# Kernel tuning notes

Hardware: AMD Instinct MI355X
Metric: run time of the kernel (lower is better)

The kernel has to match this reference:

```python
import jax, jax.numpy as jnp
import numpy as np

S, T, B = 128, 64, 64          # src_len, trg_len, batch
E, H, D, A, V = 512, 512, 1024, 256, 32000  # emb, enc_hid, dec_hid(=2H), attn, vocab
PAD = 0


def _p(key, shape, scale=0.02):
    return jax.random.normal(key, shape, dtype=jnp.float32) * scale


def setup_inputs() -> dict:
    key = jax.random.key(0)
    ks = jax.random.split(key, 20)
    return {
        'src': jax.random.randint(ks[0], (S, B), 0, V, dtype=jnp.int32),
        'trg': jax.random.randint(ks[1], (T, B), 0, V, dtype=jnp.int32),
        'enc_emb': _p(ks[2], (V, E)),
        'Wf_ih': _p(ks[3], (4 * H, E)), 'Wf_hh': _p(ks[4], (4 * H, H)), 'bf': jnp.zeros((4 * H,), jnp.float32),
        'Wb_ih': _p(ks[5], (4 * H, E)), 'Wb_hh': _p(ks[6], (4 * H, H)), 'bb': jnp.zeros((4 * H,), jnp.float32),
        'Wa': _p(ks[7], (A, 2 * H + D)), 'ba': jnp.zeros((A,), jnp.float32),
        'v': _p(ks[8], (A,)),
        'dec_emb': _p(ks[9], (V, E)),
        'Wd_ih': _p(ks[10], (4 * D, E + 2 * H)), 'Wd_hh': _p(ks[11], (4 * D, D)), 'bd': jnp.zeros((4 * D,), jnp.float32),
        'Wo': _p(ks[12], (V, 2 * H + D + E)), 'bo': jnp.zeros((V,), jnp.float32),
    }


def lstm_cell(x, h, c, W_ih, W_hh, b):
    # PyTorch gate order: i, f, g, o
    g = x @ W_ih.T + h @ W_hh.T + b
    i, f, gg, o = jnp.split(g, 4, axis=-1)
    c2 = jax.nn.sigmoid(f) * c + jax.nn.sigmoid(i) * jnp.tanh(gg)
    h2 = jax.nn.sigmoid(o) * jnp.tanh(c2)
    return h2, c2


def seq2seq_fwd(src, trg, enc_emb, Wf_ih, Wf_hh, bf, Wb_ih, Wb_hh, bb,
                Wa, ba, v, dec_emb, Wd_ih, Wd_hh, bd, Wo, bo):
    emb = enc_emb[src]                                   # [S,B,E]
    z = jnp.zeros((B, H), emb.dtype)

    def fstep(carry, x):
        h, c = lstm_cell(x, *carry, Wf_ih, Wf_hh, bf)
        return (h, c), h

    def bstep(carry, x):
        h, c = lstm_cell(x, *carry, Wb_ih, Wb_hh, bb)
        return (h, c), h

    (hf, cf), hs_f = jax.lax.scan(fstep, (z, z), emb)
    (hb, cb), hs_b = jax.lax.scan(bstep, (z, z), emb[::-1])
    enc_out = jnp.concatenate([hs_f, hs_b[::-1]], axis=-1)   # [S,B,2H]

    h0 = jnp.concatenate([hf, hb], axis=-1)              # [B,D]
    c0 = jnp.concatenate([cf, cb], axis=-1)

    mask = (src != PAD).T                                # [B,S]
    enc_bse = enc_out.transpose(1, 0, 2)                 # [B,S,2H]

    def dstep(carry, tok):
        h, c = carry
        emb_t = dec_emb[tok]                             # [B,E]
        hrep = jnp.broadcast_to(h[:, None, :], (B, S, D))
        energy = jnp.tanh(jnp.concatenate([hrep, enc_bse], -1) @ Wa.T + ba)  # [B,S,A]
        scores = energy @ v                              # [B,S]
        scores = jnp.where(mask, scores, jnp.float32(-1e10))
        a = jax.nn.softmax(scores, axis=1)
        ctx = jnp.einsum('bs,bse->be', a, enc_bse)       # [B,2H]
        x = jnp.concatenate([emb_t, ctx], axis=-1)
        h2, c2 = lstm_cell(x, h, c, Wd_ih, Wd_hh, bd)
        pred = jnp.concatenate([h2, ctx, emb_t], -1) @ Wo.T + bo  # [B,V]
        return (h2, c2), pred

    # teacher_forcing_ratio = 1.0 -> input at step t is trg[t-1]
    _, preds = jax.lax.scan(dstep, (h0, c0), trg[:-1])
    outputs = jnp.concatenate([jnp.zeros((1, B, V), preds.dtype), preds], axis=0)
    return outputs                                       # [T,B,V]


def reference(src, trg, enc_emb, Wf_ih, Wf_hh, bf, Wb_ih, Wb_hh, bb,
              Wa, ba, v, dec_emb, Wd_ih, Wd_hh, bd, Wo, bo):
    return seq2seq_fwd(src, trg, enc_emb, Wf_ih, Wf_hh, bf, Wb_ih, Wb_hh, bb,
                       Wa, ba, v, dec_emb, Wd_ih, Wd_hh, bd, Wo, bo)
```

## Files before the change

kernel.cpp:

```cpp
#include <hip/hip_runtime.h>

#define SLEN  128
#define BATCH 64
#define EMB   512
#define HID   512
#define DDEC  1024
#define ATT   256
#define VOC   32000
#define TSTEPS 63
#define LINE  16

typedef _Float16 f16x4 __attribute__((ext_vector_type(4)));
typedef _Float16 f16x8 __attribute__((ext_vector_type(8)));
typedef float    f32x4 __attribute__((ext_vector_type(4)));

union HQ  { unsigned long long q[2]; f16x8 v; };
union HP  { _Float16 h[2]; unsigned u; };
union HP4 { _Float16 h[4]; f16x4 v4; unsigned long long u; };

__device__ __forceinline__ float sigmoidf_(float x) { return 1.0f / (1.0f + __expf(-x)); }
__device__ __forceinline__ float tanhf_(float x)    { return 1.0f - 2.0f / (__expf(2.0f * x) + 1.0f); }

__device__ __forceinline__ void st_u32(void* p, unsigned v) {
    __hip_atomic_store((unsigned*)p, v, __ATOMIC_RELAXED, __HIP_MEMORY_SCOPE_AGENT);
}
__device__ __forceinline__ void st_u64(void* p, unsigned long long v) {
    __hip_atomic_store((unsigned long long*)p, v, __ATOMIC_RELAXED, __HIP_MEMORY_SCOPE_AGENT);
}
__device__ __forceinline__ unsigned long long ld_u64(const void* p) {
    return __hip_atomic_load((const unsigned long long*)p, __ATOMIC_RELAXED, __HIP_MEMORY_SCOPE_AGENT);
}

__device__ __forceinline__ void barx(int* base, int leaf, int perleaf, int nleaf) {
    __syncthreads();
    if (threadIdx.x == 0) {
        int* lc = base + leaf * LINE;
        int* lg = base + (16 + leaf) * LINE;
        int* rc = base + 32 * LINE;
        int* rg = base + 33 * LINE;
        int g = __hip_atomic_load(lg, __ATOMIC_RELAXED, __HIP_MEMORY_SCOPE_AGENT);
        int prev = __hip_atomic_fetch_add(lc, 1, __ATOMIC_RELAXED, __HIP_MEMORY_SCOPE_AGENT);
        if (prev == perleaf - 1) {
            __hip_atomic_store(lc, 0, __ATOMIC_RELAXED, __HIP_MEMORY_SCOPE_AGENT);
            int rgen = __hip_atomic_load(rg, __ATOMIC_RELAXED, __HIP_MEMORY_SCOPE_AGENT);
            int rprev = __hip_atomic_fetch_add(rc, 1, __ATOMIC_RELAXED, __HIP_MEMORY_SCOPE_AGENT);
            if (rprev == nleaf - 1) {
                __hip_atomic_store(rc, 0, __ATOMIC_RELAXED, __HIP_MEMORY_SCOPE_AGENT);
                __hip_atomic_store(rg, rgen + 1, __ATOMIC_RELAXED, __HIP_MEMORY_SCOPE_AGENT);
            } else {
                while (__hip_atomic_load(rg, __ATOMIC_RELAXED, __HIP_MEMORY_SCOPE_AGENT) == rgen)
                    __builtin_amdgcn_s_sleep(1);
            }
            __hip_atomic_store(lg, g + 1, __ATOMIC_RELAXED, __HIP_MEMORY_SCOPE_AGENT);
        } else {
            while (__hip_atomic_load(lg, __ATOMIC_RELAXED, __HIP_MEMORY_SCOPE_AGENT) == g)
                __builtin_amdgcn_s_sleep(1);
        }
    }
    __syncthreads();
}

__global__ __launch_bounds__(256) void init_convert(
    const int* __restrict__ src, const int* __restrict__ trg,
    const float* __restrict__ enc_emb, const float* __restrict__ dec_emb,
    const float* __restrict__ Wf_ih, const float* __restrict__ Wf_hh,
    const float* __restrict__ Wb_ih, const float* __restrict__ Wb_hh,
    const float* __restrict__ Wa, const float* __restrict__ Wd_ih, const float* __restrict__ Wd_hh,
    float* __restrict__ out0,
    _Float16* __restrict__ Wenc16, _Float16* __restrict__ Wd16, _Float16* __restrict__ Wa16,
    _Float16* __restrict__ emb_src16, _Float16* __restrict__ predA,
    float* __restrict__ c_enc, _Float16* __restrict__ h16_enc, int* __restrict__ bar_ws)
{
    long idx = (long)blockIdx.x * 256 + threadIdx.x;
    if (idx < 2048000L) { out0[idx] = 0.f; return; }
    idx -= 2048000L;
    if (idx < 4194304L) {
        int dir = (int)(idx >> 21);
        int rem = (int)(idx & ((1 << 21) - 1));
        int rr = rem >> 10, c = rem & 1023;
        int d = rr >> 2, qg = rr & 3;
        const float* Wih = dir ? Wb_ih : Wf_ih;
        const float* Whh = dir ? Wb_hh : Wf_hh;
        float v = (c < 512) ? Wih[(long)(qg * 512 + d) * 512 + c]
                            : Whh[(long)(qg * 512 + d) * 512 + (c - 512)];
        Wenc16[idx] = (_Float16)v; return;
    }
    idx -= 4194304L;
    if (idx < 10485760L) {
        int rr = (int)(idx / 2560), c = (int)(idx % 2560);
        int d = rr >> 2, qg = rr & 3;
        float v = (c < 1536) ? Wd_ih[(long)(qg * 1024 + d) * 1536 + c]
                             : Wd_hh[(long)(qg * 1024 + d) * 1024 + (c - 1536)];
        Wd16[idx] = (_Float16)v; return;
    }
    idx -= 10485760L;
    if (idx < 262144L) {
        int rr = (int)(idx >> 10), c = (int)(idx & 1023);
        Wa16[idx] = (_Float16)Wa[(long)rr * 2048 + c]; return;
    }
    idx -= 262144L;
    if (idx < 4194304L) {
        int sb = (int)(idx >> 9), e = (int)(idx & 511);
        int tok = src[sb];
        emb_src16[idx] = (_Float16)enc_emb[(long)tok * 512 + e]; return;
    }
    idx -= 4194304L;
    if (idx < 2064384L) {
        int rI = (int)(idx >> 9), e = (int)(idx & 511);
        int tok = trg[rI];
        predA[(long)(64 + rI) * 2560 + 2048 + e] = (_Float16)dec_emb[(long)tok * 512 + e]; return;
    }
    idx -= 2064384L;
    if (idx < 65536L) { c_enc[idx] = 0.f; return; }
    idx -= 65536L;
    if (idx < 65536L) { h16_enc[idx] = (_Float16)0.f; return; }
    idx -= 65536L;
    if (idx < 2048L) { bar_ws[idx] = 0; }
}

__global__ __launch_bounds__(256, 1) void enc_coop(
    const _Float16* __restrict__ Wenc16, const _Float16* __restrict__ emb_src16,
    _Float16* __restrict__ h16_enc, float* __restrict__ c_enc,
    const float* __restrict__ bf, const float* __restrict__ bb,
    _Float16* __restrict__ enc_out16, int* __restrict__ bar_ws)
{
    __shared__ _Float16 Wl[16384];
    __shared__ float gbuf[16][65];

    const int t = threadIdx.x, lane = t & 63, w = t >> 6;
    const int blk = blockIdx.x, dir = blk >> 7, tile = blk & 127;
    const int r16 = lane & 15, kg = lane >> 4;
    int* bar_base = bar_ws + dir * 34 * LINE;
    const int leaf = tile & 15;

    #pragma unroll
    for (int i = 0; i < 8; ++i) {
        int h0 = (i * 256 + t) * 8;
        int kc = h0 >> 9, l = (h0 >> 3) & 63;
        f16x8 v = *(const f16x8*)(Wenc16 + ((size_t)(dir * 2048 + tile * 16 + (l & 15))) * 1024 + (l >> 4) * 8 + kc * 32);
        *(f16x8*)&Wl[h0] = v;
    }

    const float* bias = dir ? bb : bf;
    const int pb = t & 63, pp = (t >> 6) & 1;
    float bias2[2][4];
    float creg2[2] = {0.f, 0.f};
    if (t < 128) {
        #pragma unroll
        for (int j = 0; j < 2; ++j)
            #pragma unroll
            for (int q = 0; q < 4; ++q)
                bias2[j][q] = bias[q * 512 + tile * 4 + pp * 2 + j];
    }
    __syncthreads();

    for (int s = 0; s < SLEN; ++s) {
        const int par = s & 1;
        const int s_eff = dir ? (127 - s) : s;
        const _Float16* Ax = emb_src16 + ((size_t)(s_eff * 64 + w * 16 + r16)) * 512 + kg * 8;
        const unsigned long long* Hq =
            (const unsigned long long*)(h16_enc + ((size_t)((par * 2 + dir) * 64 + w * 16 + r16)) * 512);
        f32x4 a0 = {}, a1 = {};
        #pragma unroll 8
        for (int kc = 0; kc < 16; ++kc) {
            f16x8 bx = *(const f16x8*)&Wl[kc * 512 + lane * 8];
            f16x8 ax = *(const f16x8*)(Ax + kc * 32);
            a0 = __builtin_amdgcn_mfma_f32_16x16x32_f16(ax, bx, a0, 0, 0, 0);
            f16x8 bh = *(const f16x8*)&Wl[(16 + kc) * 512 + lane * 8];
            HQ hq;
            hq.q[0] = ld_u64(Hq + kc * 8 + kg * 2);
            hq.q[1] = ld_u64(Hq + kc * 8 + kg * 2 + 1);
            a1 = __builtin_amdgcn_mfma_f32_16x16x32_f16(hq.v, bh, a1, 0, 0, 0);
        }
        #pragma unroll
        for (int rI = 0; rI < 4; ++rI)
            gbuf[r16][w * 16 + kg * 4 + rI] = a0[rI] + a1[rI];
        __syncthreads();
        if (t < 128) {
            HP hp;
            #pragma unroll
            for (int j = 0; j < 2; ++j) {
                const int dl = pp * 2 + j;
                float g0 = gbuf[dl * 4 + 0][pb] + bias2[j][0];
                float g1 = gbuf[dl * 4 + 1][pb] + bias2[j][1];
                float g2 = gbuf[dl * 4 + 2][pb] + bias2[j][2];
                float g3 = gbuf[dl * 4 + 3][pb] + bias2[j][3];
                float c2 = sigmoidf_(g1) * creg2[j] + sigmoidf_(g0) * tanhf_(g2);
                float h2 = sigmoidf_(g3) * tanhf_(c2);
                creg2[j] = c2;
                hp.h[j] = (_Float16)h2;
            }
            const int d0 = tile * 4 + pp * 2;
            st_u32((void*)(h16_enc + ((size_t)((par ^ 1) * 2 + dir) * 64 + pb) * 512 + d0), hp.u);
            *(unsigned*)(enc_out16 + ((size_t)s_eff * 64 + pb) * 1024 + dir * 512 + d0) = hp.u;
        }
        barx(bar_base, leaf, 8, 16);
    }
    if (t < 128) {
        const int d0 = tile * 4 + pp * 2;
        c_enc[((size_t)dir * 64 + pb) * 512 + d0] = creg2[0];
        c_enc[((size_t)dir * 64 + pb) * 512 + d0 + 1] = creg2[1];
    }
}

__global__ __launch_bounds__(256, 1) void dec_coop(
    const _Float16* __restrict__ Wd16, const _Float16* __restrict__ Wa16,
    const float* __restrict__ bd, const float* __restrict__ vvec,
    const int* __restrict__ src, const _Float16* __restrict__ enc_part16,
    const _Float16* __restrict__ enc_out16, const float* __restrict__ c_enc,
    _Float16* __restrict__ predA, int* __restrict__ bar_ws)
{
    __shared__ _Float16 Wl[40960];
    __shared__ float gbuf[16][65];
    __shared__ float ha[256], sv[256], sc[128], red[128];

    const int t = threadIdx.x, lane = t & 63, w = t >> 6;
    const int tile = blockIdx.x;
    const int r16 = lane & 15, kg = lane >> 4;
    int* bar_base = bar_ws + 2 * 34 * LINE;
    const int leaf = tile & 15;

    #pragma unroll
    for (int i = 0; i < 20; ++i) {
        int h0 = (i * 256 + t) * 8;
        int kc = h0 >> 9, l = (h0 >> 3) & 63;
        f16x8 v = *(const f16x8*)(Wd16 + ((size_t)(tile * 16 + (l & 15))) * 2560 + (l >> 4) * 8 + kc * 32);
        *(f16x8*)&Wl[h0] = v;
    }

    const int pb = t & 63, pp = (t >> 6) & 1;
    float bias2[2][4], creg2[2] = {0.f, 0.f};
    if (t < 128) {
        #pragma unroll
        for (int j = 0; j < 2; ++j) {
            const int dg = tile * 4 + pp * 2 + j;
            #pragma unroll
            for (int q = 0; q < 4; ++q) bias2[j][q] = bd[q * 1024 + dg];
            creg2[j] = (dg < 512) ? c_enc[(size_t)pb * 512 + dg]
                                  : c_enc[(size_t)(64 + pb) * 512 + (dg - 512)];
        }
    }

    const int b0 = blockIdx.x;
    if (b0 < 64) {
        sv[t] = vvec[t];
        #pragma unroll
        for (int i = 0; i < 2; ++i) {
            int pidx = i * 256 + t;
            int d = pidx * 2;
            const size_t rbase = (d < 512) ? (size_t)(127 * 64 + b0) * 1024 : (size_t)(0 * 64 + b0) * 1024;
            HP hp;
            hp.h[0] = enc_out16[rbase + d];
            hp.h[1] = enc_out16[rbase + d + 1];
            st_u32((void*)(predA + (size_t)b0 * 2560 + d), hp.u);
        }
    }
    barx(bar_base, leaf, 16, 16);

    for (int tt = 0; tt < TSTEPS; ++tt) {
        if (b0 < 64) {
            const int base_m = b0 & 48;
            const _Float16* Ahh = predA + ((size_t)(tt * 64 + base_m + r16)) * 2560 + kg * 8;
            f32x4 acc4[4] = {};
            #pragma unroll 4
            for (int kc = 0; kc < 32; ++kc) {
                f16x8 a = *(const f16x8*)(Ahh + kc * 32);
                #pragma unroll
                for (int jj = 0; jj < 4; ++jj) {
                    f16x8 bw = *(const f16x8*)(Wa16 + ((size_t)((w * 4 + jj) * 16 + r16)) * 1024 + kg * 8 + kc * 32);
                    acc4[jj] = __builtin_amdgcn_mfma_f32_16x16x32_f16(a, bw, acc4[jj], 0, 0, 0);
                }
            }
            if (kg == ((b0 & 15) >> 2)) {
                #pragma unroll
                for (int jj = 0; jj < 4; ++jj)
                    ha[(w * 4 + jj) * 16 + r16] = acc4[jj][b0 & 3];
            }
            __syncthreads();
            if (t < 128) {
                const f16x8* ep = (const f16x8*)(enc_part16 + ((size_t)t * 64 + b0) * 256);
                float acc = 0.f;
                #pragma unroll 4
                for (int j8 = 0; j8 < 32; ++j8) {
                    f16x8 e = ep[j8];
                    #pragma unroll
                    for (int u = 0; u < 8; ++u)
                        acc += tanhf_(ha[j8 * 8 + u] + (float)e[u]) * sv[j8 * 8 + u];
                }
                float scv = (src[t * 64 + b0] != 0) ? acc : -1e10f;
                sc[t] = scv; red[t] = scv;
            }
            __syncthreads();
            for (int off = 64; off > 0; off >>= 1) { if (t < off) red[t] = fmaxf(red[t], red[t + off]); __syncthreads(); }
            const float mx = red[0];
            __syncthreads();
            if (t < 128) { float e = __expf(sc[t] - mx); sc[t] = e; red[t] = e; }
            __syncthreads();
            for (int off = 64; off > 0; off >>= 1) { if (t < off) red[t] += red[t + off]; __syncthreads(); }
            const float inv = 1.0f / red[0];
            __syncthreads();
            float a0 = 0.f, a1 = 0.f, a2 = 0.f, a3 = 0.f;
            for (int sI = 0; sI < 128; ++sI) {
                float as = sc[sI] * inv;
                f16x4 ev = *(const f16x4*)(enc_out16 + ((size_t)sI * 64 + b0) * 1024 + t * 4);
                a0 += as * (float)ev[0]; a1 += as * (float)ev[1];
                a2 += as * (float)ev[2]; a3 += as * (float)ev[3];
            }
            HP4 o;
            o.h[0] = (_Float16)a0; o.h[1] = (_Float16)a1;
            o.h[2] = (_Float16)a2; o.h[3] = (_Float16)a3;
            st_u64((void*)(predA + ((size_t)(64 + tt * 64 + b0)) * 2560 + 1024 + t * 4), o.u);
        }
        barx(bar_base, leaf, 16, 16);
        {
            const _Float16* Ae = predA + ((size_t)(64 + tt * 64 + w * 16 + r16)) * 2560 + kg * 8;
            const _Float16* Ah = predA + ((size_t)(tt * 64 + w * 16 + r16)) * 2560 + kg * 8;
            f32x4 ae = {}, ac = {}, ah = {};
            #pragma unroll 8
            for (int kc = 0; kc < 16; ++kc) {
                f16x8 bw = *(const f16x8*)&Wl[kc * 512 + lane * 8];
                f16x8 a = *(const f16x8*)(Ae + 2048 + kc * 32);
                ae = __builtin_amdgcn_mfma_f32_16x16x32_f16(a, bw, ae, 0, 0, 0);
            }
            #pragma unroll 8
            for (int kc = 0; kc < 32; ++kc) {
                f16x8 bw = *(const f16x8*)&Wl[(16 + kc) * 512 + lane * 8];
                f16x8 a = *(const f16x8*)(Ae + 1024 + kc * 32);
                ac = __builtin_amdgcn_mfma_f32_16x16x32_f16(a, bw, ac, 0, 0, 0);
            }
            #pragma unroll 8
            for (int kc = 0; kc < 32; ++kc) {
                f16x8 bw = *(const f16x8*)&Wl[(48 + kc) * 512 + lane * 8];
                f16x8 a = *(const f16x8*)(Ah + kc * 32);
                ah = __builtin_amdgcn_mfma_f32_16x16x32_f16(a, bw, ah, 0, 0, 0);
            }
            #pragma unroll
            for (int rI = 0; rI < 4; ++rI)
                gbuf[r16][w * 16 + kg * 4 + rI] = ae[rI] + ac[rI] + ah[rI];
            __syncthreads();
            if (t < 128) {
                HP hp;
                #pragma unroll
                for (int j = 0; j < 2; ++j) {
                    const int dl = pp * 2 + j;
                    float g0 = gbuf[dl * 4 + 0][pb] + bias2[j][0];
                    float g1 = gbuf[dl * 4 + 1][pb] + bias2[j][1];
                    float g2 = gbuf[dl * 4 + 2][pb] + bias2[j][2];
                    float g3 = gbuf[dl * 4 + 3][pb] + bias2[j][3];
                    float c2 = sigmoidf_(g1) * creg2[j] + sigmoidf_(g0) * tanhf_(g2);
                    float h2 = sigmoidf_(g3) * tanhf_(c2);
                    creg2[j] = c2;
                    hp.h[j] = (_Float16)h2;
                }
                st_u32((void*)(predA + ((size_t)(64 + tt * 64 + pb)) * 2560 + tile * 4 + pp * 2), hp.u);
            }
        }
        barx(bar_base, leaf, 16, 16);
    }
}

__global__ __launch_bounds__(64) void enc_step_mfma(
    const _Float16* __restrict__ Wenc16, const _Float16* __restrict__ emb_src16,
    _Float16* __restrict__ h16_enc, float* __restrict__ c_enc,
    const float* __restrict__ bf, const float* __restrict__ bb,
    _Float16* __restrict__ enc_out16, int s)
{
    __shared__ float gbuf[16 * 66];
    const int lane = threadIdx.x;
    const int blk = blockIdx.x;
    const int dir = blk >> 7, tile = blk & 127;
    const int par = s & 1;
    const int s_eff = dir ? (SLEN - 1 - s) : s;
    const int r16 = lane & 15, kg = lane >> 4;

    const _Float16* Bw = Wenc16 + ((size_t)(dir * 2048 + tile * 16 + r16)) * 1024 + kg * 8;
    const _Float16* Ax = emb_src16 + ((size_t)(s_eff * 64 + r16)) * 512 + kg * 8;
    const _Float16* Ah = h16_enc + ((size_t)((par * 2 + dir) * 64 + r16)) * 512 + kg * 8;

    f32x4 acc[4] = {};
    #pragma unroll 4
    for (int kc = 0; kc < 16; ++kc) {
        f16x8 bfr = *(const f16x8*)(Bw + kc * 32);
        #pragma unroll
        for (int m = 0; m < 4; ++m) {
            f16x8 a = *(const f16x8*)(Ax + kc * 32 + (size_t)m * 16 * 512);
            acc[m] = __builtin_amdgcn_mfma_f32_16x16x32_f16(a, bfr, acc[m], 0, 0, 0);
        }
    }
    #pragma unroll 4
    for (int kc = 0; kc < 16; ++kc) {
        f16x8 bfr = *(const f16x8*)(Bw + 512 + kc * 32);
        #pragma unroll
        for (int m = 0; m < 4; ++m) {
            f16x8 a = *(const f16x8*)(Ah + kc * 32 + (size_t)m * 16 * 512);
            acc[m] = __builtin_amdgcn_mfma_f32_16x16x32_f16(a, bfr, acc[m], 0, 0, 0);
        }
    }
    #pragma unroll
    for (int m = 0; m < 4; ++m)
        #pragma unroll
        for (int rI = 0; rI < 4; ++rI)
            gbuf[r16 * 66 + m * 16 + kg * 4 + rI] = acc[m][rI];
    __syncthreads();

    const float* bias = dir ? bb : bf;
    const int b = lane;
    #pragma unroll
    for (int dl = 0; dl < 4; ++dl) {
        const int d = tile * 4 + dl;
        float g0 = gbuf[(dl * 4 + 0) * 66 + b] + bias[d];
        float g1 = gbuf[(dl * 4 + 1) * 66 + b] + bias[512 + d];
        float g2 = gbuf[(dl * 4 + 2) * 66 + b] + bias[1024 + d];
        float g3 = gbuf[(dl * 4 + 3) * 66 + b] + bias[1536 + d];
        const size_t cur = ((size_t)(par * 2 + dir) * 64 + b) * 512 + d;
        const size_t nxt = ((size_t)((par ^ 1) * 2 + dir) * 64 + b) * 512 + d;
        float c2 = sigmoidf_(g1) * c_enc[cur] + sigmoidf_(g0) * tanhf_(g2);
        float h2 = sigmoidf_(g3) * tanhf_(c2);
        c_enc[nxt] = c2;
        h16_enc[nxt] = (_Float16)h2;
        enc_out16[((size_t)s_eff * 64 + b) * 1024 + dir * 512 + d] = (_Float16)h2;
    }
}

__global__ __launch_bounds__(256) void dec_init(
    const _Float16* __restrict__ enc_out16, const float* __restrict__ c_enc,
    _Float16* __restrict__ predA, float* __restrict__ c_dec)
{
    int idx = blockIdx.x * 256 + threadIdx.x;
    int b = (idx >> 10) & 63, d = idx & 1023;
    if (idx < 65536) {
        _Float16 v = (d < 512) ? enc_out16[(size_t)(127 * 64 + b) * 1024 + d]
                               : enc_out16[(size_t)(0 * 64 + b) * 1024 + d];
        predA[(size_t)b * 2560 + d] = v;
    } else {
        float v = (d < 512) ? c_enc[((size_t)(0 * 2 + 0) * 64 + b) * 512 + d]
                            : c_enc[((size_t)(0 * 2 + 1) * 64 + b) * 512 + (d - 512)];
        c_dec[(size_t)b * 1024 + d] = v;
    }
}

__global__ __launch_bounds__(64) void hatt_mfma(
    const _Float16* __restrict__ predA, const _Float16* __restrict__ Wa16,
    float* __restrict__ hatt, int t)
{
    const int lane = threadIdx.x;
    const int tile = blockIdx.x;
    const int r16 = lane & 15, kg = lane >> 4;
    const _Float16* Ap = predA + ((size_t)(t * 64 + r16)) * 2560 + kg * 8;
    const _Float16* Bw = Wa16 + ((size_t)(tile * 16 + r16)) * 1024 + kg * 8;
    f32x4 acc[4] = {};
    #pragma unroll 4
    for (int kc = 0; kc < 32; ++kc) {
        f16x8 bfr = *(const f16x8*)(Bw + kc * 32);
        #pragma unroll
        for (int m = 0; m < 4; ++m) {
            f16x8 a = *(const f16x8*)(Ap + kc * 32 + (size_t)m * 16 * 2560);
            acc[m] = __builtin_amdgcn_mfma_f32_16x16x32_f16(a, bfr, acc[m], 0, 0, 0);
        }
    }
    #pragma unroll
    for (int m = 0; m < 4; ++m)
        #pragma unroll
        for (int rI = 0; rI < 4; ++rI)
            hatt[(size_t)(m * 16 + kg * 4 + rI) * 256 + tile * 16 + r16] = acc[m][rI];
}

__global__ __launch_bounds__(256) void attn_step(
    const int* __restrict__ src, const float* __restrict__ hatt, const float* __restrict__ vvec,
    const _Float16* __restrict__ enc_part16, const _Float16* __restrict__ enc_out16,
    _Float16* __restrict__ predA, int t)
{
    __shared__ float ha[256], sv[256], sc[128], red[128];
    const int b = blockIdx.x, tid = threadIdx.x;
    ha[tid] = hatt[b * 256 + tid];
    sv[tid] = vvec[tid];
    __syncthreads();
    if (tid < 128) {
        const f16x8* ep = (const f16x8*)(enc_part16 + ((size_t)tid * 64 + b) * 256);
        float acc = 0.f;
        #pragma unroll 4
        for (int j8 = 0; j8 < 32; ++j8) {
            f16x8 e = ep[j8];
            #pragma unroll
            for (int u = 0; u < 8; ++u)
                acc += tanhf_(ha[j8 * 8 + u] + (float)e[u]) * sv[j8 * 8 + u];
        }
        float scv = (src[tid * 64 + b] != 0) ? acc : -1e10f;
        sc[tid] = scv; red[tid] = scv;
    }
    __syncthreads();
    for (int off = 64; off > 0; off >>= 1) { if (tid < off) red[tid] = fmaxf(red[tid], red[tid + off]); __syncthreads(); }
    const float mx = red[0];
    __syncthreads();
    if (tid < 128) { float e = __expf(sc[tid] - mx); sc[tid] = e; red[tid] = e; }
    __syncthreads();
    for (int off = 64; off > 0; off >>= 1) { if (tid < off) red[tid] += red[tid + off]; __syncthreads(); }
    const float inv = 1.0f / red[0];
    __syncthreads();

    float a0 = 0.f, a1 = 0.f, a2 = 0.f, a3 = 0.f;
    for (int sI = 0; sI < 128; ++sI) {
        float as = sc[sI] * inv;
        f16x4 ev = *(const f16x4*)(enc_out16 + ((size_t)sI * 64 + b) * 1024 + tid * 4);
        a0 += as * (float)ev[0]; a1 += as * (float)ev[1];
        a2 += as * (float)ev[2]; a3 += as * (float)ev[3];
    }
    f16x4 o = { (_Float16)a0, (_Float16)a1, (_Float16)a2, (_Float16)a3 };
    *(f16x4*)(predA + ((size_t)(64 + t * 64 + b)) * 2560 + 1024 + tid * 4) = o;
}

__global__ __launch_bounds__(64) void dec_gates(
    const _Float16* __restrict__ Wd16, const float* __restrict__ bd,
    float* __restrict__ c_dec, _Float16* __restrict__ predA, int t)
{
    __shared__ float gbuf[16 * 66];
    const int lane = threadIdx.x;
    const int tile = blockIdx.x;
    const int par = t & 1;
    const int r16 = lane & 15, kg = lane >> 4;
    const _Float16* Bw = Wd16 + ((size_t)(tile * 16 + r16)) * 2560 + kg * 8;
    const _Float16* At = predA + ((size_t)(64 + t * 64 + r16)) * 2560 + kg * 8;
    const _Float16* Ah = predA + ((size_t)(t * 64 + r16)) * 2560 + kg * 8;
    f32x4 acc[4] = {};
    #pragma unroll 4
    for (int kc = 0; kc < 16; ++kc) {
        f16x8 bfr = *(const f16x8*)(Bw + kc * 32);
        #pragma unroll
        for (int m = 0; m < 4; ++m) {
            f16x8 a = *(const f16x8*)(At + 2048 + kc * 32 + (size_t)m * 16 * 2560);
            acc[m] = __builtin_amdgcn_mfma_f32_16x16x32_f16(a, bfr, acc[m], 0, 0, 0);
        }
    }
    #pragma unroll 4
    for (int kc = 0; kc < 32; ++kc) {
        f16x8 bfr = *(const f16x8*)(Bw + 512 + kc * 32);
        #pragma unroll
        for (int m = 0; m < 4; ++m) {
            f16x8 a = *(const f16x8*)(At + 1024 + kc * 32 + (size_t)m * 16 * 2560);
            acc[m] = __builtin_amdgcn_mfma_f32_16x16x32_f16(a, bfr, acc[m], 0, 0, 0);
        }
    }
    #pragma unroll 4
    for (int kc = 0; kc < 32; ++kc) {
        f16x8 bfr = *(const f16x8*)(Bw + 1536 + kc * 32);
        #pragma unroll
        for (int m = 0; m < 4; ++m) {
            f16x8 a = *(const f16x8*)(Ah + kc * 32 + (size_t)m * 16 * 2560);
            acc[m] = __builtin_amdgcn_mfma_f32_16x16x32_f16(a, bfr, acc[m], 0, 0, 0);
        }
    }
    #pragma unroll
    for (int m = 0; m < 4; ++m)
        #pragma unroll
        for (int rI = 0; rI < 4; ++rI)
            gbuf[r16 * 66 + m * 16 + kg * 4 + rI] = acc[m][rI];
    __syncthreads();

    const int b = lane;
    #pragma unroll
    for (int dl = 0; dl < 4; ++dl) {
        const int d = tile * 4 + dl;
        float g0 = gbuf[(dl * 4 + 0) * 66 + b] + bd[d];
        float g1 = gbuf[(dl * 4 + 1) * 66 + b] + bd[1024 + d];
        float g2 = gbuf[(dl * 4 + 2) * 66 + b] + bd[2048 + d];
        float g3 = gbuf[(dl * 4 + 3) * 66 + b] + bd[3072 + d];
        float c2 = sigmoidf_(g1) * c_dec[(size_t)(par * 64 + b) * 1024 + d] + sigmoidf_(g0) * tanhf_(g2);
        float h2 = sigmoidf_(g3) * tanhf_(c2);
        c_dec[(size_t)((par ^ 1) * 64 + b) * 1024 + d] = c2;
        predA[((size_t)(64 + t * 64 + b)) * 2560 + d] = (_Float16)h2;
    }
}

__global__ __launch_bounds__(256, 2) void gemm_a16(
    const _Float16* __restrict__ A, int lda,
    const float* __restrict__ B, int ldb,
    const float* __restrict__ bias,
    void* __restrict__ Cv, int ldc, int K, int Mvalid, int ntn, int c16)
{
    __shared__ _Float16 As[8192];
    __shared__ _Float16 Bs[8192];

    const int nwg = gridDim.x;
    const int id = blockIdx.x;
    const int q = nwg >> 3, r = nwg & 7;
    const int xcd = id & 7, ix = id >> 3;
    const int wg = (xcd < r) ? (xcd * (q + 1) + ix) : (r * (q + 1) + (xcd - r) * q + ix);
    const int per = ntn << 3;
    const int g = wg / per, rem = wg % per;
    const int mt = g * 8 + (rem & 7), nt = rem >> 3;

    const int t = threadIdx.x, lane = t & 63, wid = t >> 6;
    const int wr = wid >> 1, wc = wid & 1;

    const int arow_s = t >> 3, ac8 = t & 7;
    const int brow_s = t >> 4, bc4 = t & 15;
    const _Float16* Ap = A + (size_t)(mt * 128 + arow_s) * lda + ac8 * 8;
    const float*    Bp = B + (size_t)(nt * 128 + brow_s) * ldb + bc4 * 4;
    const int awx = (ac8 * 8) ^ ((arow_s & 7) << 3);
    const int bwx = (bc4 * 4) ^ ((brow_s & 7) << 3);

    const int kts = K >> 6;
    f32x4 acc[4][4] = {};
    f16x8 ra[4]; float4 rb[8];
    #pragma unroll
    for (int i = 0; i < 4; ++i) ra[i] = *(const f16x8*)(Ap + (size_t)i * 32 * lda);
    #pragma unroll
    for (int i = 0; i < 8; ++i) rb[i] = *(const float4*)(Bp + (size_t)i * 16 * ldb);

    const int abase = (wr * 64 + (lane & 15)) * 64 + (lane >> 4) * 8;
    const int bbase = (wc * 64 + (lane & 15)) * 64 + (lane >> 4) * 8;
    const int sxor = (lane & 7) << 3;

    for (int kt = 0; kt < kts; ++kt) {
        f16x4 cb[8];
        #pragma unroll
        for (int i = 0; i < 8; ++i)
            cb[i] = (f16x4){(_Float16)rb[i].x, (_Float16)rb[i].y, (_Float16)rb[i].z, (_Float16)rb[i].w};
        __syncthreads();
        #pragma unroll
        for (int i = 0; i < 4; ++i)
            *(f16x8*)&As[(arow_s + i * 32) * 64 + awx] = ra[i];
        #pragma unroll
        for (int i = 0; i < 8; ++i)
            *(f16x4*)&Bs[(brow_s + i * 16) * 64 + bwx] = cb[i];
        __syncthreads();
        if (kt + 1 < kts) {
            #pragma unroll
            for (int i = 0; i < 4; ++i) ra[i] = *(const f16x8*)(Ap + (size_t)i * 32 * lda + (kt + 1) * 64);
            #pragma unroll
            for (int i = 0; i < 8; ++i) rb[i] = *(const float4*)(Bp + (size_t)i * 16 * ldb + (kt + 1) * 64);
        }
        #pragma unroll
        for (int kk = 0; kk < 2; ++kk) {
            f16x8 af[4], bfr[4];
            #pragma unroll
            for (int m = 0; m < 4; ++m) af[m]  = *(const f16x8*)&As[(abase + m * 16 * 64 + kk * 32) ^ sxor];
            #pragma unroll
            for (int n = 0; n < 4; ++n) bfr[n] = *(const f16x8*)&Bs[(bbase + n * 16 * 64 + kk * 32) ^ sxor];
            #pragma unroll
            for (int m = 0; m < 4; ++m)
                #pragma unroll
                for (int n = 0; n < 4; ++n)
                    acc[m][n] = __builtin_amdgcn_mfma_f32_16x16x32_f16(af[m], bfr[n], acc[m][n], 0, 0, 0);
        }
    }

    const int ccol = nt * 128 + wc * 64 + (lane & 15);
    const int crow0 = mt * 128 + wr * 64 + ((lane >> 4) << 2);
    float bv[4];
    #pragma unroll
    for (int n = 0; n < 4; ++n) bv[n] = bias[ccol + n * 16];
    #pragma unroll
    for (int m = 0; m < 4; ++m) {
        #pragma unroll
        for (int rI = 0; rI < 4; ++rI) {
            const int row = crow0 + m * 16 + rI;
            if (row < Mvalid) {
                if (c16) {
                    _Float16* C = (_Float16*)Cv;
                    #pragma unroll
                    for (int n = 0; n < 4; ++n)
                        C[(size_t)row * ldc + ccol + n * 16] = (_Float16)(acc[m][n][rI] + bv[n]);
                } else {
                    float* C = (float*)Cv;
                    #pragma unroll
                    for (int n = 0; n < 4; ++n)
                        C[(size_t)row * ldc + ccol + n * 16] = acc[m][n][rI] + bv[n];
                }
            }
        }
    }
}

extern "C" void kernel_launch(void* const* d_in, const int* in_sizes, int n_in,
                              void* d_out, int out_size, void* d_ws, size_t ws_size,
                              hipStream_t stream) {
    const int*   src     = (const int*)d_in[0];
    const int*   trg     = (const int*)d_in[1];
    const float* enc_emb = (const float*)d_in[2];
    const float* Wf_ih   = (const float*)d_in[3];
    const float* Wf_hh   = (const float*)d_in[4];
    const float* bf      = (const float*)d_in[5];
    const float* Wb_ih   = (const float*)d_in[6];
    const float* Wb_hh   = (const float*)d_in[7];
    const float* bb      = (const float*)d_in[8];
    const float* Wa      = (const float*)d_in[9];
    const float* ba      = (const float*)d_in[10];
    const float* vvec    = (const float*)d_in[11];
    const float* dec_emb = (const float*)d_in[12];
    const float* Wd_ih   = (const float*)d_in[13];
    const float* Wd_hh   = (const float*)d_in[14];
    const float* bd      = (const float*)d_in[15];
    const float* Wo      = (const float*)d_in[16];
    const float* bo      = (const float*)d_in[17];
    float* out = (float*)d_out;

    char* w = (char*)d_ws;
    _Float16* Wenc16     = (_Float16*)(w);
    _Float16* Wd16       = (_Float16*)(w + 8388608);
    _Float16* Wa16       = (_Float16*)(w + 29360128);
    _Float16* emb_src16  = (_Float16*)(w + 29884416);
    _Float16* enc_out16  = (_Float16*)(w + 38273024);
    _Float16* predA      = (_Float16*)(w + 55050240);
    _Float16* h16_enc    = (_Float16*)(w + 76349440);
    float*    c_enc      = (float*)   (w + 76611584);
    float*    c_dec      = (float*)   (w + 77135872);
    float*    hatt       = (float*)   (w + 77660160);
    _Float16* enc_part16 = (_Float16*)(w + 77725696);
    int*      bar_ws     = (int*)     (w + 81920000);
    const size_t need_bytes = 81928192;
    if (ws_size < need_bytes) return;

    init_convert<<<91336, 256, 0, stream>>>(
        src, trg, enc_emb, dec_emb, Wf_ih, Wf_hh, Wb_ih, Wb_hh, Wa, Wd_ih, Wd_hh,
        out, Wenc16, Wd16, Wa16, emb_src16, predA, c_enc, h16_enc, bar_ws);

    {
        const _Float16* a0 = Wenc16; const _Float16* a1 = emb_src16;
        _Float16* a2 = h16_enc; float* a3 = c_enc;
        const float* a4 = bf; const float* a5 = bb;
        _Float16* a6 = enc_out16; int* a7 = bar_ws;
        void* args[] = { &a0, &a1, &a2, &a3, &a4, &a5, &a6, &a7 };
        hipError_t e = hipLaunchCooperativeKernel((const void*)enc_coop, dim3(256), dim3(256), args, 0, stream);
        if (e != hipSuccess) {
            for (int s = 0; s < SLEN; ++s)
                enc_step_mfma<<<256, 64, 0, stream>>>(Wenc16, emb_src16, h16_enc, c_enc, bf, bb, enc_out16, s);
        }
    }

    gemm_a16<<<128, 256, 0, stream>>>(enc_out16, 1024, Wa + 1024, 2048, ba,
                                      enc_part16, 256, 1024, 8192, 2, 1);

    {
        const _Float16* a0 = Wd16; const _Float16* a1 = Wa16;
        const float* a2 = bd; const float* a3 = vvec;
        const int* a4 = src; const _Float16* a5 = enc_part16;
        const _Float16* a6 = enc_out16; const float* a7 = c_enc;
        _Float16* a8 = predA; int* a9 = bar_ws;
        void* args[] = { &a0, &a1, &a2, &a3, &a4, &a5, &a6, &a7, &a8, &a9 };
        hipError_t e = hipLaunchCooperativeKernel((const void*)dec_coop, dim3(256), dim3(256), args, 0, stream);
        if (e != hipSuccess) {
            dec_init<<<512, 256, 0, stream>>>(enc_out16, c_enc, predA, c_dec);
            for (int t = 0; t < TSTEPS; ++t) {
                hatt_mfma<<<16, 64, 0, stream>>>(predA, Wa16, hatt, t);
                attn_step<<<64, 256, 0, stream>>>(src, hatt, vvec, enc_part16, enc_out16, predA, t);
                dec_gates<<<256, 64, 0, stream>>>(Wd16, bd, c_dec, predA, t);
            }
        }
    }

    gemm_a16<<<8000, 256, 0, stream>>>(predA + (size_t)64 * 2560, 2560, Wo, 2560, bo,
                                       out + (size_t)64 * VOC, VOC, 2560, 4032, 250, 0);
}
```

Measured before the change: 6.307 ms.

## Replace hierarchical atomic-counter grid barrier with flag-based detector barrier

Replaces the two-level fetch_add tree barrier used in the cooperative encoder and decoder kernels with a flag-array barrier. Each block writes its epoch to its own padded slot, a single detector block polls all flags in parallel with one thread per flag and then publishes a generation word, and the other blocks spin on that word. Decoder barriers that only need to wait on the 64 attention-producing blocks use a smaller arrival set. This is meant to remove atomic RMW contention and the serial two-hop latency on each recurrent step. In exchange it uses a larger barrier workspace that must be zeroed, and funnels every release through one block.

```diff
diff --git a/kernel.cpp b/kernel.cpp
--- a/kernel.cpp
+++ b/kernel.cpp
@@ -8,7 +8,7 @@
 #define ATT   256
 #define VOC   32000
 #define TSTEPS 63
-#define LINE  16
+#define SLOT  1024
 
 typedef _Float16 f16x4 __attribute__((ext_vector_type(4)));
 typedef _Float16 f16x8 __attribute__((ext_vector_type(8)));
@@ -30,31 +30,29 @@
 __device__ __forceinline__ unsigned long long ld_u64(const void* p) {
     return __hip_atomic_load((const unsigned long long*)p, __ATOMIC_RELAXED, __HIP_MEMORY_SCOPE_AGENT);
 }
-
-__device__ __forceinline__ void barx(int* base, int leaf, int perleaf, int nleaf) {
-    __syncthreads();
-    if (threadIdx.x == 0) {
-        int* lc = base + leaf * LINE;
-        int* lg = base + (16 + leaf) * LINE;
-        int* rc = base + 32 * LINE;
-        int* rg = base + 33 * LINE;
-        int g = __hip_atomic_load(lg, __ATOMIC_RELAXED, __HIP_MEMORY_SCOPE_AGENT);
-        int prev = __hip_atomic_fetch_add(lc, 1, __ATOMIC_RELAXED, __HIP_MEMORY_SCOPE_AGENT);
-        if (prev == perleaf - 1) {
-            __hip_atomic_store(lc, 0, __ATOMIC_RELAXED, __HIP_MEMORY_SCOPE_AGENT);
-            int rgen = __hip_atomic_load(rg, __ATOMIC_RELAXED, __HIP_MEMORY_SCOPE_AGENT);
-            int rprev = __hip_atomic_fetch_add(rc, 1, __ATOMIC_RELAXED, __HIP_MEMORY_SCOPE_AGENT);
-            if (rprev == nleaf - 1) {
-                __hip_atomic_store(rc, 0, __ATOMIC_RELAXED, __HIP_MEMORY_SCOPE_AGENT);
-                __hip_atomic_store(rg, rgen + 1, __ATOMIC_RELAXED, __HIP_MEMORY_SCOPE_AGENT);
-            } else {
-                while (__hip_atomic_load(rg, __ATOMIC_RELAXED, __HIP_MEMORY_SCOPE_AGENT) == rgen)
-                    __builtin_amdgcn_s_sleep(1);
-            }
-            __hip_atomic_store(lg, g + 1, __ATOMIC_RELAXED, __HIP_MEMORY_SCOPE_AGENT);
-        } else {
-            while (__hip_atomic_load(lg, __ATOMIC_RELAXED, __HIP_MEMORY_SCOPE_AGENT) == g)
-                __builtin_amdgcn_s_sleep(1);
+__device__ __forceinline__ void st_i32(int* p, int v) {
+    __hip_atomic_store(p, v, __ATOMIC_RELAXED, __HIP_MEMORY_SCOPE_AGENT);
+}
+__device__ __forceinline__ int ld_i32(const int* p) {
+    return __hip_atomic_load(p, __ATOMIC_RELAXED, __HIP_MEMORY_SCOPE_AGENT);
+}
+
+__device__ __forceinline__ void barf(int* flags, int* gen, int narr, int myid,
+                                     int epoch, bool amDet) {
+    __syncthreads();
+    if (amDet) {
+        if (threadIdx.x == 0 && myid < narr) st_i32(flags + myid * SLOT, epoch);
+        if ((int)threadIdx.x < narr) {
+            while (ld_i32(flags + threadIdx.x * SLOT) < epoch)
+                __builtin_amdgcn_s_sleep(2);
+        }
+        __syncthreads();
+        if (threadIdx.x == 0) st_i32(gen, epoch);
+    } else {
+        if (threadIdx.x == 0) {
+            if (myid < narr) st_i32(flags + myid * SLOT, epoch);
+            while (ld_i32(gen) < epoch)
+                __builtin_amdgcn_s_sleep(4);
         }
     }
     __syncthreads();
@@ -115,7 +113,7 @@
     idx -= 65536L;
     if (idx < 65536L) { h16_enc[idx] = (_Float16)0.f; return; }
     idx -= 65536L;
-    if (idx < 2048L) { bar_ws[idx] = 0; }
+    if (idx < 527360L) { bar_ws[idx] = 0; }
 }
 
 __global__ __launch_bounds__(256, 1) void enc_coop(
@@ -130,8 +128,9 @@
     const int t = threadIdx.x, lane = t & 63, w = t >> 6;
     const int blk = blockIdx.x, dir = blk >> 7, tile = blk & 127;
     const int r16 = lane & 15, kg = lane >> 4;
-    int* bar_base = bar_ws + dir * 34 * LINE;
-    const int leaf = tile & 15;
+    int* gflags = bar_ws + (257 + dir * 129) * SLOT;
+    int* ggen   = gflags + 128 * SLOT;
+    const bool amDet = (tile == 127);
 
     #pragma unroll
     for (int i = 0; i < 8; ++i) {
@@ -194,7 +193,7 @@
             st_u32((void*)(h16_enc + ((size_t)((par ^ 1) * 2 + dir) * 64 + pb) * 512 + d0), hp.u);
             *(unsigned*)(enc_out16 + ((size_t)s_eff * 64 + pb) * 1024 + dir * 512 + d0) = hp.u;
         }
-        barx(bar_base, leaf, 8, 16);
+        barf(gflags, ggen, 128, tile, s + 1, amDet);
     }
     if (t < 128) {
         const int d0 = tile * 4 + pp * 2;
@@ -217,8 +216,9 @@
     const int t = threadIdx.x, lane = t & 63, w = t >> 6;
     const int tile = blockIdx.x;
     const int r16 = lane & 15, kg = lane >> 4;
-    int* bar_base = bar_ws + 2 * 34 * LINE;
-    const int leaf = tile & 15;
+    int* gflags = bar_ws;
+    int* ggen   = gflags + 256 * SLOT;
+    const bool amDet = (tile == 255);
 
     #pragma unroll
     for (int i = 0; i < 20; ++i) {
@@ -255,7 +255,7 @@
             st_u32((void*)(predA + (size_t)b0 * 2560 + d), hp.u);
         }
     }
-    barx(bar_base, leaf, 16, 16);
+    barf(gflags, ggen, 64, tile, 1, amDet);
 
     for (int tt = 0; tt < TSTEPS; ++tt) {
         if (b0 < 64) {
@@ -311,7 +311,7 @@
             o.h[2] = (_Float16)a2; o.h[3] = (_Float16)a3;
             st_u64((void*)(predA + ((size_t)(64 + tt * 64 + b0)) * 2560 + 1024 + t * 4), o.u);
         }
-        barx(bar_base, leaf, 16, 16);
+        barf(gflags, ggen, 64, tile, 2 * tt + 2, amDet);
         {
             const _Float16* Ae = predA + ((size_t)(64 + tt * 64 + w * 16 + r16)) * 2560 + kg * 8;
             const _Float16* Ah = predA + ((size_t)(tt * 64 + w * 16 + r16)) * 2560 + kg * 8;
@@ -355,7 +355,7 @@
                 st_u32((void*)(predA + ((size_t)(64 + tt * 64 + pb)) * 2560 + tile * 4 + pp * 2), hp.u);
             }
         }
-        barx(bar_base, leaf, 16, 16);
+        barf(gflags, ggen, 256, tile, 2 * tt + 3, amDet);
     }
 }
 
@@ -708,10 +708,10 @@
     float*    hatt       = (float*)   (w + 77660160);
     _Float16* enc_part16 = (_Float16*)(w + 77725696);
     int*      bar_ws     = (int*)     (w + 81920000);
-    const size_t need_bytes = 81928192;
+    const size_t need_bytes = 84029440;
     if (ws_size < need_bytes) return;
 
-    init_convert<<<91336, 256, 0, stream>>>(
+    init_convert<<<93428, 256, 0, stream>>>(
         src, trg, enc_emb, dec_emb, Wf_ih, Wf_hh, Wb_ih, Wb_hh, Wa, Wd_ih, Wd_hh,
         out, Wenc16, Wd16, Wa16, emb_src16, predA, c_enc, h16_enc, bar_ws);
 
```

New measurement: 5.999 ms. 4.9% less time.
